# Kernel optimization log

Hardware: AMD Instinct MI355X
Metric: run time of the kernel (lower is better)

The kernel has to match this reference:

```python
import jax, jax.numpy as jnp
import numpy as np

N_NODES = 100000
N_EDGES = 1000000
HEADS = 3
NEG_SLOPE_ATTN = 0.2   # DGL EdgeGATConv default negative_slope
NEG_SLOPE_MLP = 0.01   # torch nn.LeakyReLU default


def _edge_softmax(e, dst, num_nodes):
    # softmax over incoming edges of each destination node; e: [E,H]
    m = jax.ops.segment_max(e, dst, num_segments=num_nodes)
    ex = jnp.exp(e - m[dst])
    s = jax.ops.segment_sum(ex, dst, num_segments=num_nodes)
    return ex / s[dst]


def _edge_gat(h, ef, src, dst, Wfc, Wedge, al, ar, ae, Wres, b, D):
    # Faithful to dgl.nn.EdgeGATConv (residual=True, bias=True defaults).
    N = h.shape[0]
    H = HEADS
    ft = (h @ Wfc).reshape(N, H, D)        # [N,H,D] projected node feats
    fe = (ef @ Wedge).reshape(-1, H, D)    # [E,H,D] projected edge feats
    el = jnp.einsum('nhd,hd->nh', ft, al)
    er = jnp.einsum('nhd,hd->nh', ft, ar)
    ee = jnp.einsum('ehd,hd->eh', fe, ae)
    e = jax.nn.leaky_relu(el[src] + er[dst] + ee, NEG_SLOPE_ATTN)  # [E,H]
    a = _edge_softmax(e, dst, N)                                   # [E,H]
    rst = jax.ops.segment_sum(ft[src] * a[..., None], dst, num_segments=N)
    # residual projection + bias (DGL defaults residual=True, bias=True)
    return rst + (h @ Wres).reshape(N, H, D) + b.reshape(1, H, D)


def _forward(node_feats, edge_feats,
             W1, We1, al1, ar1, ae1, Wr1, b1,
             W2, We2, al2, ar2, ae2, Wr2, b2,
             W3, We3, al3, ar3, ae3, Wr3, b3,
             L1a_w, L1a_b, L1b_w, L1b_b, L1c_w, L1c_b, L2_w, L2_b,
             src, dst):
    h1 = _edge_gat(node_feats, edge_feats, src, dst, W1, We1, al1, ar1, ae1, Wr1, b1, 8)
    h2 = _edge_gat(h1.mean(axis=1), edge_feats, src, dst, W2, We2, al2, ar2, ae2, Wr2, b2, 16)
    h3 = _edge_gat(h2.mean(axis=1), edge_feats, src, dst, W3, We3, al3, ar3, ae3, Wr3, b3, 32)
    # linear1 MLP head applied per (node, head)
    x = jax.nn.leaky_relu(h3 @ L1a_w + L1a_b, NEG_SLOPE_MLP)   # [N,H,16]
    x = jax.nn.leaky_relu(x @ L1b_w + L1b_b, NEG_SLOPE_MLP)    # [N,H,4]
    x = x @ L1c_w + L1c_b                                       # [N,H,1]
    x = x.reshape(x.shape[0], -1) @ L2_w + L2_b                 # [N,1]
    return jnp.max(x, axis=0)                                   # [1]


def setup_inputs() -> dict:
    key = jax.random.key(0)
    ks = iter(jax.random.split(key, 64))

    def nrm(shape, scale=0.1):
        return jax.random.normal(next(ks), shape, dtype=jnp.float32) * scale

    inp = {
        'node_feats': jax.random.normal(next(ks), (N_NODES, 6), dtype=jnp.float32),
        'edge_feats': jax.random.uniform(next(ks), (N_EDGES, 1), dtype=jnp.float32),
    }
    dims = [(6, 8), (8, 16), (16, 32)]
    for i, (din, dout) in enumerate(dims, start=1):
        inp[f'W{i}'] = nrm((din, HEADS * dout))
        inp[f'We{i}'] = nrm((1, HEADS * dout))
        inp[f'al{i}'] = nrm((HEADS, dout))
        inp[f'ar{i}'] = nrm((HEADS, dout))
        inp[f'ae{i}'] = nrm((HEADS, dout))
        inp[f'Wr{i}'] = nrm((din, HEADS * dout))
        inp[f'b{i}'] = nrm((HEADS * dout,))
    inp['L1a_w'] = nrm((32, 16)); inp['L1a_b'] = nrm((16,))
    inp['L1b_w'] = nrm((16, 4));  inp['L1b_b'] = nrm((4,))
    inp['L1c_w'] = nrm((4, 1));   inp['L1c_b'] = nrm((1,))
    inp['L2_w'] = nrm((HEADS, 1)); inp['L2_b'] = nrm((1,))
    inp['src'] = jax.random.randint(next(ks), (N_EDGES,), 0, N_NODES, dtype=jnp.int32)
    inp['dst'] = jax.random.randint(next(ks), (N_EDGES,), 0, N_NODES, dtype=jnp.int32)
    return inp


def reference(node_feats, edge_feats,
              W1, We1, al1, ar1, ae1, Wr1, b1,
              W2, We2, al2, ar2, ae2, Wr2, b2,
              W3, We3, al3, ar3, ae3, Wr3, b3,
              L1a_w, L1a_b, L1b_w, L1b_b, L1c_w, L1c_b, L2_w, L2_b,
              src, dst):
    return _forward(node_feats, edge_feats,
                    W1, We1, al1, ar1, ae1, Wr1, b1,
                    W2, We2, al2, ar2, ae2, Wr2, b2,
                    W3, We3, al3, ar3, ae3, Wr3, b3,
                    L1a_w, L1a_b, L1b_w, L1b_b, L1c_w, L1c_b, L2_w, L2_b,
                    src, dst)
```

## Files before the change

kernel.cpp:

```cpp
#include <hip/hip_runtime.h>
#include <hip/hip_fp16.h>
#include <math.h>

#define NN 100000
#define NE 1000000
#define NCHUNK 160
#define CHUNK (NE/NCHUNK)
#define NODE_RANGE (NN/8)
#define CAPS 32

typedef unsigned int   u32;
typedef unsigned short u16;

__device__ __forceinline__ float lrelu(float x, float sl){ return x >= 0.f ? x : sl*x; }

__device__ __forceinline__ void atomicMaxF(float* a, float v){
    if (v >= 0.f) atomicMax((int*)a, __float_as_int(v));
    else          atomicMin((unsigned int*)a, __float_as_uint(v));
}

__global__ void __launch_bounds__(256) kInit(int* __restrict__ deg, float* __restrict__ out){
    int i = blockIdx.x*256 + threadIdx.x;
    if (i < NN + 1) deg[i] = 0;
    if (i == 0) out[0] = -INFINITY;
}

__global__ void __launch_bounds__(256) kScatterX1(const int* __restrict__ src,
        const int* __restrict__ dst, const float* __restrict__ ef,
        int* __restrict__ deg, u32* __restrict__ pack,
        int* __restrict__ ovfc, int4* __restrict__ ovf){
    const int xcd  = blockIdx.x & 7;
    const int base = (blockIdx.x >> 3)*CHUNK;
    for (int e = base + threadIdx.x; e < base + CHUNK; e += 256){
        int d = __builtin_nontemporal_load(dst + e);
        if (d / NODE_RANGE == xcd){
            int s   = __builtin_nontemporal_load(src + e);
            float fv = __builtin_nontemporal_load(ef + e);
            int pos = atomicAdd(&deg[d], 1);
            if (pos < CAPS){
                u32 rec = ((u32)s << 15) | (u32)(fv*32767.f + 0.5f);
                pack[(size_t)d*CAPS + pos] = rec;
            } else {
                int o = atomicAdd(ovfc, 1);
                ovf[o] = make_int4(d, s, __float_as_int(fv), 0);
            }
        }
    }
}

template<int DIN, int DINP, int D, bool WRM>
__device__ void coefBody(const float* __restrict__ Wfc, const float* __restrict__ al,
                         const float* __restrict__ ar, const float* __restrict__ We,
                         const float* __restrict__ ae, const float* __restrict__ Wres,
                         const float* __restrict__ bias,
                         float* __restrict__ q, float* __restrict__ r, float* __restrict__ ce,
                         float* __restrict__ wrm, float* __restrict__ bm){
    int t = threadIdx.x;
    for (int i = t; i < 3*DINP; i += 256){
        int hd = i/DINP, k = i - hd*DINP;
        float qa = 0.f, ra = 0.f;
        if (k < DIN){
            for (int d = 0; d < D; ++d){
                float w = Wfc[k*3*D + hd*D + d];
                qa += w*al[hd*D+d];
                ra += w*ar[hd*D+d];
            }
        }
        q[i] = qa; r[i] = ra;
    }
    if (t < 3){
        float c = 0.f;
        for (int d = 0; d < D; ++d) c += We[t*D+d]*ae[t*D+d];
        ce[t] = c;
    }
    if (WRM){
        for (int i = t; i < DIN*D; i += 256){
            int k = i/D, d = i - k*D;
            wrm[i] = (Wres[k*3*D+d] + Wres[k*3*D+D+d] + Wres[k*3*D+2*D+d])*(1.f/3.f);
        }
        for (int i = t; i < D; i += 256)
            bm[i] = (bias[i] + bias[D+i] + bias[2*D+i])*(1.f/3.f);
    }
}

__global__ void __launch_bounds__(256) kPrep(
    const float* W1, const float* al1, const float* ar1, const float* We1,
    const float* ae1, const float* Wr1, const float* b1,
    const float* W2, const float* al2, const float* ar2, const float* We2,
    const float* ae2, const float* Wr2, const float* b2,
    const float* W3, const float* al3, const float* ar3, const float* We3,
    const float* ae3, const float* Wr3, const float* b3,
    const float* L1a_w, const float* L1a_b,
    float* coef, float* FA, float* FR, float* C0,
    const float* __restrict__ nf, u32* __restrict__ ntab1, float* __restrict__ er3a)
{
    if (blockIdx.x == 0){
        coefBody<6,8,8,true>(W1, al1, ar1, We1, ae1, Wr1, b1,
            coef+0, coef+24, coef+48, coef+52, coef+100);
    } else if (blockIdx.x == 1){
        coefBody<8,8,16,true>(W2, al2, ar2, We2, ae2, Wr2, b2,
            coef+108, coef+132, coef+156, coef+160, coef+288);
    } else if (blockIdx.x == 2){
        coefBody<16,16,32,false>(W3, al3, ar3, We3, ae3, Wr3, b3,
            coef+304, coef+352, coef+400, nullptr, nullptr);
    } else if (blockIdx.x == 3){
        int t = threadIdx.x;
        for (int i = t; i < 768; i += 256){
            int hd = i >> 8, rem = i & 255;
            int k = rem >> 4, ii = rem & 15;
            float a = 0.f, r = 0.f;
            for (int d = 0; d < 32; ++d){
                float w = L1a_w[d*16 + ii];
                a += W3[k*96 + hd*32 + d]*w;
                r += Wr3[k*96 + hd*32 + d]*w;
            }
            FA[i] = a; FR[i] = r;
        }
        if (t < 48){
            int hd = t >> 4, ii = t & 15;
            float c = L1a_b[ii];
            for (int d = 0; d < 32; ++d) c += b3[hd*32 + d]*L1a_w[d*16 + ii];
            C0[t] = c;
        }
    } else {
        __shared__ float r1s[24];
        int t = threadIdx.x;
        if (t < 24){
            int hd = t >> 3, k = t & 7;
            float ra = 0.f;
            if (k < 6)
                for (int d = 0; d < 8; ++d) ra += W1[k*24 + hd*8 + d]*ar1[hd*8 + d];
            r1s[t] = ra;
        }
        __syncthreads();
        int n = (blockIdx.x - 4)*256 + t;
        if (n >= NN) return;
        float h[6];
        #pragma unroll
        for (int k = 0; k < 6; ++k) h[k] = nf[(size_t)n*6 + k];
        __half2 p0 = __floats2half2_rn(h[0], h[1]);
        __half2 p1 = __floats2half2_rn(h[2], h[3]);
        __half2 p2 = __floats2half2_rn(h[4], h[5]);
        __half2 p3 = __floats2half2_rn(0.f, 0.f);
        uint4 row;
        row.x = *(u32*)&p0; row.y = *(u32*)&p1; row.z = *(u32*)&p2; row.w = *(u32*)&p3;
        *(uint4*)(ntab1 + (size_t)n*4) = row;
        #pragma unroll
        for (int hd = 0; hd < 3; ++hd){
            float er = 0.f;
            #pragma unroll
            for (int k = 0; k < 6; ++k) er += r1s[hd*8+k]*h[k];
            er3a[(size_t)n*3+hd] = er;
        }
    }
}

template<int DINP, int DINR, int D, bool AGG>
__global__ void __launch_bounds__(256) kNode(
    const int* __restrict__ deg, const u32* __restrict__ pack,
    const int* __restrict__ ovfc, const int4* __restrict__ ovf,
    const u32* __restrict__ ntab,
    const float* __restrict__ er3, const float* __restrict__ qc,
    const float* __restrict__ cep, const float* __restrict__ hres,
    const float* __restrict__ Wfc, const float* __restrict__ Wr2,
    const float* __restrict__ b2,
    float* __restrict__ hmean_o, u32* __restrict__ ntab_next,
    float* __restrict__ er3_next, const float* __restrict__ rnext,
    float* __restrict__ agg_o)
{
    constexpr int KS   = DINP/4;
    constexpr int ROWU = DINP/2;
    constexpr int D4   = D/4;
    const int tid  = threadIdx.x;
    const int lid  = tid & 63;
    const int lane = tid & 3;
    const int n    = (blockIdx.x*256 + tid) >> 2;
    const bool alive = n < NN;

    int dg = 0;
    float e0 = 0.f, e1 = 0.f, e2 = 0.f;
    if (alive){
        dg = deg[n]; if (dg > CAPS) dg = CAPS;
        e0 = er3[(size_t)n*3+0]; e1 = er3[(size_t)n*3+1]; e2 = er3[(size_t)n*3+2];
    }
    const float c0 = cep[0], c1 = cep[1], c2 = cep[2];
    float q[3*KS];
    #pragma unroll
    for (int hd = 0; hd < 3; ++hd)
        #pragma unroll
        for (int ks = 0; ks < KS; ++ks)
            q[hd*KS+ks] = qc[hd*DINP + lane*KS + ks];

    float acc[3*KS];
    #pragma unroll
    for (int v = 0; v < 3*KS; ++v) acc[v] = 0.f;
    float s0 = 0.f, s1 = 0.f, s2 = 0.f;

    auto rowLoad = [&](int sv, u32& w0, u32& w1){
        const u32* rp = ntab + (size_t)sv*ROWU + lane*(KS/2);
        if constexpr (KS == 2){ w0 = rp[0]; w1 = 0u; }
        else { uint2 t2 = *(const uint2*)rp; w0 = t2.x; w1 = t2.y; }
    };
    auto edgeCompute = [&](float fv, u32 w0, u32 w1){
        float hv[KS];
        float2 f = __half22float2(*(__half2*)&w0);
        hv[0] = f.x; hv[1] = f.y;
        if constexpr (KS == 4){
            f = __half22float2(*(__half2*)&w1);
            hv[2] = f.x; hv[3] = f.y;
        }
        float l0 = 0.f, l1 = 0.f, l2 = 0.f;
        #pragma unroll
        for (int ks = 0; ks < KS; ++ks){
            l0 += q[ks]*hv[ks]; l1 += q[KS+ks]*hv[ks]; l2 += q[2*KS+ks]*hv[ks];
        }
        l0 += __shfl_xor(l0,1); l0 += __shfl_xor(l0,2);
        l1 += __shfl_xor(l1,1); l1 += __shfl_xor(l1,2);
        l2 += __shfl_xor(l2,1); l2 += __shfl_xor(l2,2);
        float x0 = __expf(lrelu(l0 + e0 + c0*fv, 0.2f));
        float x1 = __expf(lrelu(l1 + e1 + c1*fv, 0.2f));
        float x2 = __expf(lrelu(l2 + e2 + c2*fv, 0.2f));
        s0 += x0; s1 += x1; s2 += x2;
        #pragma unroll
        for (int ks = 0; ks < KS; ++ks){
            acc[ks]      += x0*hv[ks];
            acc[KS+ks]   += x1*hv[ks];
            acc[2*KS+ks] += x2*hv[ks];
        }
    };

    int p = n*CAPS;
    const int re = p + dg;
    while (p + 1 < re){
        u32 ra = pack[p], rb = pack[p+1];
        u32 a0, a1, b0, b1;
        rowLoad((int)(ra >> 15), a0, a1);
        rowLoad((int)(rb >> 15), b0, b1);
        edgeCompute((float)(ra & 0x7fffu)*(1.f/32767.f), a0, a1);
        edgeCompute((float)(rb & 0x7fffu)*(1.f/32767.f), b0, b1);
        p += 2;
    }
    if (p < re){
        u32 ra = pack[p];
        u32 a0, a1;
        rowLoad((int)(ra >> 15), a0, a1);
        edgeCompute((float)(ra & 0x7fffu)*(1.f/32767.f), a0, a1);
    }

    int nov = ovfc[0];
    for (int i = 0; i < nov; ++i){
        int4 o = ovf[i];
        if (alive && o.x == n){
            u32 a0, a1;
            rowLoad(o.y, a0, a1);
            edgeCompute(__int_as_float(o.z), a0, a1);
        }
    }

    float i0 = s0 > 0.f ? 1.f/s0 : 0.f;
    float i1 = s1 > 0.f ? 1.f/s1 : 0.f;
    float i2 = s2 > 0.f ? 1.f/s2 : 0.f;
    if constexpr (!AGG){ i0 *= (1.f/3.f); i1 *= (1.f/3.f); i2 *= (1.f/3.f); }
    #pragma unroll
    for (int ks = 0; ks < KS; ++ks){
        acc[ks] *= i0; acc[KS+ks] *= i1; acc[2*KS+ks] *= i2;
    }

    if constexpr (AGG){
        if (alive){
            #pragma unroll
            for (int hd = 0; hd < 3; ++hd){
                float4 v = make_float4(acc[hd*KS+0], acc[hd*KS+1], acc[hd*KS+2], acc[hd*KS+3]);
                *(float4*)(agg_o + (size_t)n*48 + hd*16 + lane*4) = v;
            }
        }
        return;
    } else {
        float hsl[KS];
        #pragma unroll
        for (int ks = 0; ks < KS; ++ks){
            int k = lane*KS + ks;
            hsl[ks] = (alive && k < DINR) ? hres[(size_t)n*DINR + k] : 0.f;
        }
        float hm[D4];
        #pragma unroll
        for (int i = 0; i < D4; ++i) hm[i] = b2[lane*D4 + i];
        #pragma unroll
        for (int r = 0; r < 4; ++r){
            int sl = (lid & ~3) | ((lid + r) & 3);
            int kb = ((lane + r) & 3)*KS;
            float as[3*KS], hs[KS];
            #pragma unroll
            for (int v = 0; v < 3*KS; ++v) as[v] = __shfl(acc[v], sl);
            #pragma unroll
            for (int v = 0; v < KS; ++v) hs[v] = __shfl(hsl[v], sl);
            #pragma unroll
            for (int ks = 0; ks < KS; ++ks){
                int k = kb + ks;
                if (DINP == DINR || k < DINR){
                    #pragma unroll
                    for (int i = 0; i < D4; ++i){
                        int d = lane*D4 + i;
                        hm[i] += as[ks]     *Wfc[k*3*D + d]
                               + as[KS+ks]  *Wfc[k*3*D + D + d]
                               + as[2*KS+ks]*Wfc[k*3*D + 2*D + d]
                               + hs[ks]     *Wr2[k*D + d];
                    }
                }
            }
        }
        if (alive){
            #pragma unroll
            for (int i = 0; i < D4; ++i)
                hmean_o[(size_t)n*D + lane*D4 + i] = hm[i];
            #pragma unroll
            for (int w = 0; w < D4/2; ++w){
                __half2 hh = __floats2half2_rn(hm[2*w], hm[2*w+1]);
                ntab_next[(size_t)n*(D/2) + lane*(D4/2) + w] = *(u32*)&hh;
            }
        }
        float p0 = 0.f, p1 = 0.f, p2 = 0.f;
        #pragma unroll
        for (int i = 0; i < D4; ++i){
            int d = lane*D4 + i;
            p0 += rnext[0*D + d]*hm[i];
            p1 += rnext[1*D + d]*hm[i];
            p2 += rnext[2*D + d]*hm[i];
        }
        p0 += __shfl_xor(p0,1); p0 += __shfl_xor(p0,2);
        p1 += __shfl_xor(p1,1); p1 += __shfl_xor(p1,2);
        p2 += __shfl_xor(p2,1); p2 += __shfl_xor(p2,2);
        if (alive && lane < 3){
            float v = (lane == 0) ? p0 : ((lane == 1) ? p1 : p2);
            er3_next[(size_t)n*3 + lane] = v;
        }
    }
}

__global__ void __launch_bounds__(256) kFin3(
    const float* __restrict__ agg,
    const float* __restrict__ hres,
    const float* __restrict__ FAg, const float* __restrict__ FRg,
    const float* __restrict__ C0g,
    const float* __restrict__ L1b_w, const float* __restrict__ L1b_b,
    const float* __restrict__ L1c_w, const float* __restrict__ L1c_b,
    const float* __restrict__ L2_w, const float* __restrict__ L2_b,
    float* __restrict__ out)
{
    const int tid = threadIdx.x;
    const int n = blockIdx.x*256 + tid;
    float y = -INFINITY;
    if (n < NN){
        float hr[16];
        const float4* hr4 = (const float4*)(hres + (size_t)n*16);
        #pragma unroll
        for (int w = 0; w < 4; ++w){
            float4 v = hr4[w];
            hr[4*w]=v.x; hr[4*w+1]=v.y; hr[4*w+2]=v.z; hr[4*w+3]=v.w;
        }
        float acc = L2_b[0];
        for (int hd = 0; hd < 3; ++hd){
            float ag[16];
            const float4* ag4 = (const float4*)(agg + (size_t)n*48 + hd*16);
            #pragma unroll
            for (int w = 0; w < 4; ++w){
                float4 v = ag4[w];
                ag[4*w]=v.x; ag[4*w+1]=v.y; ag[4*w+2]=v.z; ag[4*w+3]=v.w;
            }
            float x1[16];
            #pragma unroll
            for (int i = 0; i < 16; ++i) x1[i] = C0g[hd*16 + i];
            #pragma unroll
            for (int k = 0; k < 16; ++k){
                const float a = ag[k], h = hr[k];
                const float* fap = FAg + hd*256 + k*16;
                const float* frp = FRg + hd*256 + k*16;
                #pragma unroll
                for (int i = 0; i < 16; ++i)
                    x1[i] += a*fap[i] + h*frp[i];
            }
            #pragma unroll
            for (int i = 0; i < 16; ++i) x1[i] = lrelu(x1[i], 0.01f);
            float x2[4];
            #pragma unroll
            for (int ii = 0; ii < 4; ++ii){
                float a = L1b_b[ii];
                #pragma unroll
                for (int i = 0; i < 16; ++i) a += x1[i]*L1b_w[i*4+ii];
                x2[ii] = lrelu(a, 0.01f);
            }
            float v = L1c_b[0];
            #pragma unroll
            for (int ii = 0; ii < 4; ++ii) v += x2[ii]*L1c_w[ii];
            acc += v*L2_w[hd];
        }
        y = acc;
    }
    __shared__ float red[256];
    red[tid] = y;
    __syncthreads();
    for (int o = 128; o > 0; o >>= 1){
        if (tid < o) red[tid] = fmaxf(red[tid], red[tid+o]);
        __syncthreads();
    }
    if (tid == 0) atomicMaxF(out, red[0]);
}

extern "C" void kernel_launch(void* const* d_in, const int* in_sizes, int n_in,
                              void* d_out, int out_size, void* d_ws, size_t ws_size,
                              hipStream_t stream) {
    const float* nf  = (const float*)d_in[0];
    const float* ef  = (const float*)d_in[1];
    const float* W1  = (const float*)d_in[2];
    const float* We1 = (const float*)d_in[3];
    const float* al1 = (const float*)d_in[4];
    const float* ar1 = (const float*)d_in[5];
    const float* ae1 = (const float*)d_in[6];
    const float* Wr1 = (const float*)d_in[7];
    const float* b1  = (const float*)d_in[8];
    const float* W2  = (const float*)d_in[9];
    const float* We2 = (const float*)d_in[10];
    const float* al2 = (const float*)d_in[11];
    const float* ar2 = (const float*)d_in[12];
    const float* ae2 = (const float*)d_in[13];
    const float* Wr2 = (const float*)d_in[14];
    const float* b2  = (const float*)d_in[15];
    const float* W3  = (const float*)d_in[16];
    const float* We3 = (const float*)d_in[17];
    const float* al3 = (const float*)d_in[18];
    const float* ar3 = (const float*)d_in[19];
    const float* ae3 = (const float*)d_in[20];
    const float* Wr3 = (const float*)d_in[21];
    const float* b3  = (const float*)d_in[22];
    const float* L1a_w = (const float*)d_in[23];
    const float* L1a_b = (const float*)d_in[24];
    const float* L1b_w = (const float*)d_in[25];
    const float* L1b_b = (const float*)d_in[26];
    const float* L1c_w = (const float*)d_in[27];
    const float* L1c_b = (const float*)d_in[28];
    const float* L2_w  = (const float*)d_in[29];
    const float* L2_b  = (const float*)d_in[30];
    const int* src = (const int*)d_in[31];
    const int* dst = (const int*)d_in[32];
    float* out = (float*)d_out;

    float* ws = (float*)d_ws;
    u32* ntab1 = (u32*)ws;
    u32* ntab2 = ntab1 + (size_t)NN*4;
    u32* ntab3 = ntab2 + (size_t)NN*4;
    float* f   = (float*)(ntab3 + (size_t)NN*8);
    float* hm2  = f;  f += (size_t)NN*8;
    float* hm3  = f;  f += (size_t)NN*16;
    float* aggb = f;  f += (size_t)NN*48;
    float* er3a = f;  f += (size_t)NN*3;
    float* er3b = f;  f += (size_t)NN*3;
    float* coef = f;  f += 512;
    float* FAb = f;  f += 768;
    float* FRb = f;  f += 768;
    float* C0b = f;  f += 64;
    int* deg  = (int*)f;
    int* ovfc = deg + NN;
    int4* ovf = (int4*)(ovfc + 4);
    u32* pack = (u32*)(ovf + 4096);

    const int gI = (NN + 1 + 255)/256;
    const int gX = NCHUNK*8;
    const int gPr = 4 + (NN + 255)/256;
    const int gN = (NN + 255)/256;
    const int gT = (NN*4 + 255)/256;

    kInit<<<gI,256,0,stream>>>(deg, out);

    kScatterX1<<<gX,256,0,stream>>>(src, dst, ef, deg, pack, ovfc, ovf);

    kPrep<<<gPr,256,0,stream>>>(W1, al1, ar1, We1, ae1, Wr1, b1,
                                W2, al2, ar2, We2, ae2, Wr2, b2,
                                W3, al3, ar3, We3, ae3, Wr3, b3,
                                L1a_w, L1a_b, coef, FAb, FRb, C0b,
                                nf, ntab1, er3a);

    kNode<8,6,8,false><<<gT,256,0,stream>>>(deg, pack, ovfc, ovf, ntab1, er3a,
        coef+0, coef+48, nf, W1, coef+52, coef+100,
        hm2, ntab2, er3b, coef+132, nullptr);

    kNode<8,8,16,false><<<gT,256,0,stream>>>(deg, pack, ovfc, ovf, ntab2, er3b,
        coef+108, coef+156, hm2, W2, coef+160, coef+288,
        hm3, ntab3, er3a, coef+352, nullptr);

    kNode<16,16,32,true><<<gT,256,0,stream>>>(deg, pack, ovfc, ovf, ntab3, er3a,
        coef+304, coef+400, hm3, W3, nullptr, nullptr,
        nullptr, nullptr, nullptr, nullptr, aggb);

    kFin3<<<gN,256,0,stream>>>(aggb, hm3, FAb, FRb, C0b,
        L1b_w, L1b_b, L1c_w, L1c_b, L2_w, L2_b, out);
}
```

Measured before the change: 179.2 us.

## Fuse edge scatter into prep kernel with vectorized 4-edge loads

Result: no change. 178.0 us (-0.6%).

```diff
diff --git a/kernel.cpp b/kernel.cpp
--- a/kernel.cpp
+++ b/kernel.cpp
@@ -4,13 +4,13 @@
 
 #define NN 100000
 #define NE 1000000
-#define NCHUNK 160
-#define CHUNK (NE/NCHUNK)
 #define NODE_RANGE (NN/8)
 #define CAPS 32
-
-typedef unsigned int   u32;
-typedef unsigned short u16;
+#define GX 2048
+
+typedef unsigned int        u32;
+typedef unsigned short      u16;
+typedef long long           s64;
 
 __device__ __forceinline__ float lrelu(float x, float sl){ return x >= 0.f ? x : sl*x; }
 
@@ -23,29 +23,6 @@
     int i = blockIdx.x*256 + threadIdx.x;
     if (i < NN + 1) deg[i] = 0;
     if (i == 0) out[0] = -INFINITY;
-}
-
-__global__ void __launch_bounds__(256) kScatterX1(const int* __restrict__ src,
-        const int* __restrict__ dst, const float* __restrict__ ef,
-        int* __restrict__ deg, u32* __restrict__ pack,
-        int* __restrict__ ovfc, int4* __restrict__ ovf){
-    const int xcd  = blockIdx.x & 7;
-    const int base = (blockIdx.x >> 3)*CHUNK;
-    for (int e = base + threadIdx.x; e < base + CHUNK; e += 256){
-        int d = __builtin_nontemporal_load(dst + e);
-        if (d / NODE_RANGE == xcd){
-            int s   = __builtin_nontemporal_load(src + e);
-            float fv = __builtin_nontemporal_load(ef + e);
-            int pos = atomicAdd(&deg[d], 1);
-            if (pos < CAPS){
-                u32 rec = ((u32)s << 15) | (u32)(fv*32767.f + 0.5f);
-                pack[(size_t)d*CAPS + pos] = rec;
-            } else {
-                int o = atomicAdd(ovfc, 1);
-                ovf[o] = make_int4(d, s, __float_as_int(fv), 0);
-            }
-        }
-    }
 }
 
 template<int DIN, int DINP, int D, bool WRM>
@@ -83,7 +60,11 @@
     }
 }
 
-__global__ void __launch_bounds__(256) kPrep(
+__global__ void __launch_bounds__(256) kScatPrep(
+    const int* __restrict__ src, const int* __restrict__ dst,
+    const float* __restrict__ ef,
+    int* __restrict__ deg, u32* __restrict__ pack,
+    int* __restrict__ ovfc, int4* __restrict__ ovf,
     const float* W1, const float* al1, const float* ar1, const float* We1,
     const float* ae1, const float* Wr1, const float* b1,
     const float* W2, const float* al2, const float* ar2, const float* We2,
@@ -94,16 +75,50 @@
     float* coef, float* FA, float* FR, float* C0,
     const float* __restrict__ nf, u32* __restrict__ ntab1, float* __restrict__ er3a)
 {
-    if (blockIdx.x == 0){
+    if (blockIdx.x < GX){
+        const int xcd = blockIdx.x & 7;
+        const int stride = (GX >> 3)*1024;
+        for (int e0 = (blockIdx.x >> 3)*1024 + threadIdx.x*4; e0 < NE; e0 += stride){
+            s64 a = __builtin_nontemporal_load((const s64*)(dst + e0));
+            s64 b = __builtin_nontemporal_load((const s64*)(dst + e0) + 1);
+            int d0 = (int)a, d1 = (int)(a >> 32), d2 = (int)b, d3 = (int)(b >> 32);
+            bool m0 = (d0/NODE_RANGE == xcd), m1 = (d1/NODE_RANGE == xcd);
+            bool m2 = (d2/NODE_RANGE == xcd), m3 = (d3/NODE_RANGE == xcd);
+            if (!(m0|m1|m2|m3)) continue;
+            s64 sa = *((const s64*)(src + e0));
+            s64 sb = *((const s64*)(src + e0) + 1);
+            float4 f4 = *(const float4*)(ef + e0);
+            int s0 = (int)sa, s1 = (int)(sa >> 32), s2 = (int)sb, s3 = (int)(sb >> 32);
+            #define DO_EDGE(mj, dj, sj, fj)                                          \
+                if (mj){                                                             \
+                    int pos = atomicAdd(&deg[dj], 1);                                \
+                    if (pos < CAPS)                                                  \
+                        pack[(size_t)(dj)*CAPS + pos] =                              \
+                            ((u32)(sj) << 15) | (u32)((fj)*32767.f + 0.5f);          \
+                    else {                                                           \
+                        int o = atomicAdd(ovfc, 1);                                  \
+                        ovf[o] = make_int4(dj, sj, __float_as_int(fj), 0);           \
+                    }                                                                \
+                }
+            DO_EDGE(m0, d0, s0, f4.x)
+            DO_EDGE(m1, d1, s1, f4.y)
+            DO_EDGE(m2, d2, s2, f4.z)
+            DO_EDGE(m3, d3, s3, f4.w)
+            #undef DO_EDGE
+        }
+        return;
+    }
+    const int bid = blockIdx.x - GX;
+    if (bid == 0){
         coefBody<6,8,8,true>(W1, al1, ar1, We1, ae1, Wr1, b1,
             coef+0, coef+24, coef+48, coef+52, coef+100);
-    } else if (blockIdx.x == 1){
+    } else if (bid == 1){
         coefBody<8,8,16,true>(W2, al2, ar2, We2, ae2, Wr2, b2,
             coef+108, coef+132, coef+156, coef+160, coef+288);
-    } else if (blockIdx.x == 2){
+    } else if (bid == 2){
         coefBody<16,16,32,false>(W3, al3, ar3, We3, ae3, Wr3, b3,
             coef+304, coef+352, coef+400, nullptr, nullptr);
-    } else if (blockIdx.x == 3){
+    } else if (bid == 3){
         int t = threadIdx.x;
         for (int i = t; i < 768; i += 256){
             int hd = i >> 8, rem = i & 255;
@@ -133,7 +148,7 @@
             r1s[t] = ra;
         }
         __syncthreads();
-        int n = (blockIdx.x - 4)*256 + t;
+        int n = (bid - 4)*256 + t;
         if (n >= NN) return;
         float h[6];
         #pragma unroll
@@ -463,21 +478,19 @@
     int4* ovf = (int4*)(ovfc + 4);
     u32* pack = (u32*)(ovf + 4096);
 
-    const int gI = (NN + 1 + 255)/256;
-    const int gX = NCHUNK*8;
-    const int gPr = 4 + (NN + 255)/256;
-    const int gN = (NN + 255)/256;
-    const int gT = (NN*4 + 255)/256;
+    const int gI  = (NN + 1 + 255)/256;
+    const int gSP = GX + 4 + (NN + 255)/256;
+    const int gN  = (NN + 255)/256;
+    const int gT  = (NN*4 + 255)/256;
 
     kInit<<<gI,256,0,stream>>>(deg, out);
 
-    kScatterX1<<<gX,256,0,stream>>>(src, dst, ef, deg, pack, ovfc, ovf);
-
-    kPrep<<<gPr,256,0,stream>>>(W1, al1, ar1, We1, ae1, Wr1, b1,
-                                W2, al2, ar2, We2, ae2, Wr2, b2,
-                                W3, al3, ar3, We3, ae3, Wr3, b3,
-                                L1a_w, L1a_b, coef, FAb, FRb, C0b,
-                                nf, ntab1, er3a);
+    kScatPrep<<<gSP,256,0,stream>>>(src, dst, ef, deg, pack, ovfc, ovf,
+                                    W1, al1, ar1, We1, ae1, Wr1, b1,
+                                    W2, al2, ar2, We2, ae2, Wr2, b2,
+                                    W3, al3, ar3, We3, ae3, Wr3, b3,
+                                    L1a_w, L1a_b, coef, FAb, FRb, C0b,
+                                    nf, ntab1, er3a);
 
     kNode<8,6,8,false><<<gT,256,0,stream>>>(deg, pack, ovfc, ovf, ntab1, er3a,
         coef+0, coef+48, nf, W1, coef+52, coef+100,
```
